# Kernel optimization log

Hardware: AMD Instinct MI355X
Metric: run time of the kernel (lower is better)

## Reference

```python
import jax, jax.numpy as jnp
import numpy as np

V, E, H, L, S, B = 32000, 512, 1024, 2, 512, 32


def setup_inputs() -> dict:
    key = jax.random.key(0)
    ks = jax.random.split(key, 12)
    s = 0.05  # keep activations in a sane range
    return {
        "x": jax.random.randint(ks[0], (S, B), 0, V),
        "embed": jax.random.normal(ks[1], (V, E), dtype=jnp.float32) * s,
        "W_ih0": jax.random.normal(ks[2], (4 * H, E), dtype=jnp.float32) * s,
        "W_hh0": jax.random.normal(ks[3], (4 * H, H), dtype=jnp.float32) * s,
        "b_ih0": jax.random.normal(ks[4], (4 * H,), dtype=jnp.float32) * s,
        "b_hh0": jax.random.normal(ks[5], (4 * H,), dtype=jnp.float32) * s,
        "W_ih1": jax.random.normal(ks[6], (4 * H, H), dtype=jnp.float32) * s,
        "W_hh1": jax.random.normal(ks[7], (4 * H, H), dtype=jnp.float32) * s,
        "b_ih1": jax.random.normal(ks[8], (4 * H,), dtype=jnp.float32) * s,
        "b_hh1": jax.random.normal(ks[9], (4 * H,), dtype=jnp.float32) * s,
        "h0": jax.random.normal(ks[10], (L, B, H), dtype=jnp.float32) * s,
        "c0": jax.random.normal(ks[11], (L, B, H), dtype=jnp.float32) * s,
    }


def _lstm_cell(x_t, h_prev, c_prev, Wi, Wh, bi, bh):
    # PyTorch gate order: input, forget, cell(g), output
    gates = x_t @ Wi.T + h_prev @ Wh.T + bi + bh  # [B, 4H]
    i, f, g, o = jnp.split(gates, 4, axis=-1)
    i = jax.nn.sigmoid(i)
    f = jax.nn.sigmoid(f)
    g = jnp.tanh(g)
    o = jax.nn.sigmoid(o)
    c_new = f * c_prev + i * g
    h_new = o * jnp.tanh(c_new)
    return h_new, c_new


def reference(x, embed, W_ih0, W_hh0, b_ih0, b_hh0,
              W_ih1, W_hh1, b_ih1, b_hh1, h0, c0):
    emb = embed[x]  # [S, B, E]; dropout p=0.0 -> identity
    layers = ((W_ih0, W_hh0, b_ih0, b_hh0), (W_ih1, W_hh1, b_ih1, b_hh1))

    def step(carry, e_t):
        h, c = carry  # each [L, B, H]
        inp = e_t
        new_h, new_c = [], []
        for l, (Wi, Wh, bi, bh) in enumerate(layers):
            h_l, c_l = _lstm_cell(inp, h[l], c[l], Wi, Wh, bi, bh)
            new_h.append(h_l)
            new_c.append(c_l)
            inp = h_l  # inter-layer dropout p=0.0 -> identity
        h = jnp.stack(new_h)
        c = jnp.stack(new_c)
        return (h, c), (inp, h, c)

    (_, _), (outs, hiddens, cells) = jax.lax.scan(step, (h0, c0), emb)
    outputs = outs[:, None, :, :]  # match torch shape [S, 1, B, H]
    return outputs, hiddens, cells
```

## Files before the change

kernel.cpp:

```cpp
#include <hip/hip_runtime.h>
#include <hip/hip_cooperative_groups.h>

namespace cg = cooperative_groups;


#define S_LEN 512
#define BATCH 32
#define HID   1024
#define EMB   512
#define NBLK  128
#define NTHR  512

typedef short  bf16x8 __attribute__((ext_vector_type(8)));
typedef float  f32x4  __attribute__((ext_vector_type(4)));

union U8 { bf16x8 v; unsigned short us[8]; uint4 u4; unsigned long long ull[2]; };

__device__ __forceinline__ unsigned short f2bf(float f) {
    unsigned u = __float_as_uint(f);
    u += 0x7fffu + ((u >> 16) & 1u);
    return (unsigned short)(u >> 16);
}

__device__ __forceinline__ uint4 pack8(float4 lo, float4 hi) {
    U8 r;
    r.us[0] = f2bf(lo.x); r.us[1] = f2bf(lo.y); r.us[2] = f2bf(lo.z); r.us[3] = f2bf(lo.w);
    r.us[4] = f2bf(hi.x); r.us[5] = f2bf(hi.y); r.us[6] = f2bf(hi.z); r.us[7] = f2bf(hi.w);
    return r.u4;
}

__device__ __forceinline__ f32x4 mfma16(bf16x8 a, bf16x8 b, f32x4 c) {
    return __builtin_amdgcn_mfma_f32_16x16x32_bf16(a, b, c, 0, 0, 0);
}

__device__ __forceinline__ U8 ld_ws16(const uint4* p) {
    const unsigned long long* q = (const unsigned long long*)p;
    U8 r;
    r.ull[0] = __hip_atomic_load(q,     __ATOMIC_RELAXED, __HIP_MEMORY_SCOPE_AGENT);
    r.ull[1] = __hip_atomic_load(q + 1, __ATOMIC_RELAXED, __HIP_MEMORY_SCOPE_AGENT);
    return r;
}
__device__ __forceinline__ void st_ws16(uint4* p, U8 v) {
    unsigned long long* q = (unsigned long long*)p;
    __hip_atomic_store(q,     v.ull[0], __ATOMIC_RELAXED, __HIP_MEMORY_SCOPE_AGENT);
    __hip_atomic_store(q + 1, v.ull[1], __ATOMIC_RELAXED, __HIP_MEMORY_SCOPE_AGENT);
}

__device__ __forceinline__ float sigm(float x) {
    return __builtin_amdgcn_rcpf(1.0f + __expf(-x));
}
__device__ __forceinline__ float tanh_fast(float x) {
    const float xc = fminf(fmaxf(x, -15.f), 15.f);
    const float t  = __expf(2.f * xc);
    return (t - 1.f) * __builtin_amdgcn_rcpf(t + 1.f);
}

__device__ __forceinline__ void poll64(const int* flags, int target) {
    const int* p = flags + ((threadIdx.x & 63) << 4);
    for (;;) {
        const int v = __hip_atomic_load(p, __ATOMIC_RELAXED, __HIP_MEMORY_SCOPE_AGENT);
        if (__all(v >= target)) break;
        __builtin_amdgcn_s_sleep(1);
    }
}

__global__ __launch_bounds__(NTHR, 1)
void lstm_pipe(const int* __restrict__ x, const float* __restrict__ embed,
               const float* __restrict__ Wi0, const float* __restrict__ Wh0,
               const float* __restrict__ bi0, const float* __restrict__ bh0,
               const float* __restrict__ Wi1, const float* __restrict__ Wh1,
               const float* __restrict__ bi1, const float* __restrict__ bh1,
               const float* __restrict__ h0in, const float* __restrict__ c0in,
               float* __restrict__ outputs, float* __restrict__ hiddens,
               float* __restrict__ cells, uint4* __restrict__ ws)
{
    __shared__ f32x4 sRed[8][8][64];
    __shared__ float sGates[32][68];
    __shared__ unsigned short sHex[32][16];
    __shared__ float sBias[16][4];
    uint4* sEmb = (uint4*)&sRed[0][0][0];

    const int tid  = threadIdx.x;
    const int lane = tid & 63;
    const int wv   = tid >> 6;
    const int bx   = blockIdx.x;
    const bool isL0 = (bx < 64);
    const int g    = isL0 ? bx : bx - 64;

    uint4* h0base = ws;
    uint4* h1base = ws + 16384;
    int*   fbase  = (int*)(ws + 24576);
    int*   flag0  = fbase;
    int*   flag1  = fbase + 1024;

    {
        const int gt = bx * NTHR + tid;
        if (gt < 2048) fbase[gt] = 0;
        if (gt < 8192) {
            const int layer = gt >> 12, kg = (gt >> 5) & 127, b = gt & 31;
            const float* src = h0in + (((size_t)layer << 5) + b) * HID + (kg << 3);
            uint4* dst = layer ? (h1base + 4096) : (h0base + 3 * 4096);
            dst[(kg << 5) + b] = pack8(*(const float4*)src, *(const float4*)(src + 4));
        }
    }
    if (tid < 16) {
        #pragma unroll
        for (int gate = 0; gate < 4; ++gate) {
            const int r = (gate << 10) + (g << 4) + tid;
            sBias[tid][gate] = isL0 ? (bi0[r] + bh0[r]) : (bi1[r] + bh1[r]);
        }
    }
    const int pjj = tid & 15;
    const int pb  = tid >> 4;
    const int jg  = (g << 4) + pjj;
    float creg = isL0 ? c0in[(size_t)pb * HID + jg]
                      : c0in[(size_t)(BATCH + pb) * HID + jg];

    const int n_    = lane & 15;
    const int ko_   = (lane >> 4) << 3;
    const int rb_   = ((n_ >> 2) << 10) + (g << 4) + (n_ & 3);
    bf16x8 w0[4][6];
    bf16x8 w1[4][8];
    if (isL0) {
        #pragma unroll
        for (int nt = 0; nt < 4; ++nt) {
            const int r = rb_ + (nt << 2);
            #pragma unroll
            for (int kf = 0; kf < 6; ++kf) {
                const int k = wv * 192 + kf * 32 + ko_;
                const float* src = (k < EMB) ? Wi0 + (size_t)r * EMB + k
                                             : Wh0 + (size_t)r * HID + (k - EMB);
                U8 t; t.u4 = pack8(*(const float4*)src, *(const float4*)(src + 4));
                w0[nt][kf] = t.v;
            }
        }
    } else {
        #pragma unroll
        for (int nt = 0; nt < 4; ++nt) {
            const int r = rb_ + (nt << 2);
            #pragma unroll
            for (int kf = 0; kf < 8; ++kf) {
                const int k = (wv << 8) + kf * 32 + ko_;
                const float* src = (k < HID) ? Wi1 + (size_t)r * HID + k
                                             : Wh1 + (size_t)r * HID + (k - HID);
                U8 t; t.u4 = pack8(*(const float4*)src, *(const float4*)(src + 4));
                w1[nt][kf] = t.v;
            }
        }
    }

    float4 pe[4][2];
    if (isL0) {
        #pragma unroll
        for (int it = 0; it < 4; ++it) {
            const int b = wv + (it << 3);
            const float* src = embed + (size_t)x[b] * EMB + (lane << 3);
            pe[it][0] = *(const float4*)src;
            pe[it][1] = *(const float4*)(src + 4);
        }
    }

    cg::grid_group grid = cg::this_grid();
    grid.sync();

    const size_t BH = (size_t)BATCH * HID;

    if (isL0) {
        for (int s = 0; s < S_LEN; ++s) {
            #pragma unroll
            for (int it = 0; it < 4; ++it)
                sEmb[lane * 33 + wv + (it << 3)] = pack8(pe[it][0], pe[it][1]);
            __syncthreads();

            if (s + 1 < S_LEN) {
                #pragma unroll
                for (int it = 0; it < 4; ++it) {
                    const int b = wv + (it << 3);
                    const float* src = embed + (size_t)x[((s + 1) << 5) + b] * EMB + (lane << 3);
                    pe[it][0] = *(const float4*)src;
                    pe[it][1] = *(const float4*)(src + 4);
                }
            }
            if (wv >= 2) poll64(flag0, s);

            const uint4* h0p = h0base + (((s + 3) & 3) << 12);

            U8 r0[6], r1[6];
            #pragma unroll
            for (int kf = 0; kf < 6; ++kf) {
                const int kfg = wv * 6 + kf;
                if (kfg >= 16) {
                    const int u = (((kfg - 16) << 2) + (lane >> 4)) * 32 + (lane & 15);
                    r0[kf] = ld_ws16(&h0p[u]);
                    r1[kf] = ld_ws16(&h0p[u + 16]);
                }
            }
            f32x4 acc[2][4] = {{{0,0,0,0},{0,0,0,0},{0,0,0,0},{0,0,0,0}},
                               {{0,0,0,0},{0,0,0,0},{0,0,0,0},{0,0,0,0}}};
            #pragma unroll
            for (int kf = 0; kf < 6; ++kf) {
                const int kfg = wv * 6 + kf;
                bf16x8 a0, a1;
                if (kfg < 16) {
                    const int u = ((kfg << 2) + (lane >> 4)) * 33 + (lane & 15);
                    U8 t0; t0.u4 = sEmb[u];      a0 = t0.v;
                    U8 t1; t1.u4 = sEmb[u + 16]; a1 = t1.v;
                } else {
                    a0 = r0[kf].v;
                    a1 = r1[kf].v;
                }
                #pragma unroll
                for (int nt = 0; nt < 4; ++nt) {
                    acc[0][nt] = mfma16(a0, w0[nt][kf], acc[0][nt]);
                    acc[1][nt] = mfma16(a1, w0[nt][kf], acc[1][nt]);
                }
            }
            __syncthreads();
            #pragma unroll
            for (int mt = 0; mt < 2; ++mt)
                #pragma unroll
                for (int nt = 0; nt < 4; ++nt)
                    sRed[wv][(mt << 2) + nt][lane] = acc[mt][nt];
            __syncthreads();
            {
                const int tile = tid >> 6, l = tid & 63;
                f32x4 sum = sRed[0][tile][l];
                #pragma unroll
                for (int w = 1; w < 8; ++w) sum += sRed[w][tile][l];
                const int mt = tile >> 2, nt = tile & 3;
                const int b0 = (mt << 4) + ((l >> 4) << 2);
                const int col = (nt << 4) + (l & 15);
                sGates[b0 + 0][col] = sum[0];
                sGates[b0 + 1][col] = sum[1];
                sGates[b0 + 2][col] = sum[2];
                sGates[b0 + 3][col] = sum[3];
            }
            __syncthreads();
            float cn_out, hn_out;
            {
                const int cb = ((pjj >> 2) << 4) + (pjj & 3);
                const float ii = sigm     (sGates[pb][cb]      + sBias[pjj][0]);
                const float ff = sigm     (sGates[pb][cb + 4]  + sBias[pjj][1]);
                const float gg = tanh_fast(sGates[pb][cb + 8]  + sBias[pjj][2]);
                const float oo = sigm     (sGates[pb][cb + 12] + sBias[pjj][3]);
                cn_out = ff * creg + ii * gg;
                creg = cn_out;
                hn_out = oo * tanh_fast(cn_out);
                sHex[pb][pjj] = f2bf(hn_out);
            }
            __syncthreads();
            if (wv == 0) {
                if (s >= 4) poll64(flag1, s - 3);
                const int b = lane & 31, kgl = lane >> 5;
                U8 hb;
                #pragma unroll
                for (int jj = 0; jj < 8; ++jj) hb.us[jj] = sHex[b][(kgl << 3) + jj];
                st_ws16(h0base + ((s & 3) << 12) + (((g << 1) + kgl) << 5) + b, hb);
                asm volatile("s_waitcnt vmcnt(0)" ::: "memory");
                if (lane == 0)
                    __hip_atomic_store(flag0 + (g << 4), s + 1,
                                       __ATOMIC_RELAXED, __HIP_MEMORY_SCOPE_AGENT);
            }
            cells  [(size_t)(s << 1) * BH + (size_t)pb * HID + jg] = cn_out;
            hiddens[(size_t)(s << 1) * BH + (size_t)pb * HID + jg] = hn_out;
        }
    } else {
        for (int s = 0; s < S_LEN; ++s) {
            if (wv < 4) poll64(flag0, s + 1);
            else        poll64(flag1, s);

            const uint4* h0c = h0base + ((s & 3) << 12);
            const uint4* h1p = h1base + (((s + 1) & 1) << 12);

            U8 r0[8], r1[8];
            #pragma unroll
            for (int kf = 0; kf < 8; ++kf) {
                const int kfg = (wv << 3) + kf;
                const uint4* src = (kfg < 32) ? h0c : h1p;
                const int u = (((kfg & 31) << 2) + (lane >> 4)) * 32 + (lane & 15);
                r0[kf] = ld_ws16(&src[u]);
                r1[kf] = ld_ws16(&src[u + 16]);
            }
            f32x4 acc[2][4] = {{{0,0,0,0},{0,0,0,0},{0,0,0,0},{0,0,0,0}},
                               {{0,0,0,0},{0,0,0,0},{0,0,0,0},{0,0,0,0}}};
            #pragma unroll
            for (int kf = 0; kf < 8; ++kf) {
                #pragma unroll
                for (int nt = 0; nt < 4; ++nt) {
                    acc[0][nt] = mfma16(r0[kf].v, w1[nt][kf], acc[0][nt]);
                    acc[1][nt] = mfma16(r1[kf].v, w1[nt][kf], acc[1][nt]);
                }
            }
            #pragma unroll
            for (int mt = 0; mt < 2; ++mt)
                #pragma unroll
                for (int nt = 0; nt < 4; ++nt)
                    sRed[wv][(mt << 2) + nt][lane] = acc[mt][nt];
            __syncthreads();
            {
                const int tile = tid >> 6, l = tid & 63;
                f32x4 sum = sRed[0][tile][l];
                #pragma unroll
                for (int w = 1; w < 8; ++w) sum += sRed[w][tile][l];
                const int mt = tile >> 2, nt = tile & 3;
                const int b0 = (mt << 4) + ((l >> 4) << 2);
                const int col = (nt << 4) + (l & 15);
                sGates[b0 + 0][col] = sum[0];
                sGates[b0 + 1][col] = sum[1];
                sGates[b0 + 2][col] = sum[2];
                sGates[b0 + 3][col] = sum[3];
            }
            __syncthreads();
            float cn_out, hn_out;
            {
                const int cb = ((pjj >> 2) << 4) + (pjj & 3);
                const float ii = sigm     (sGates[pb][cb]      + sBias[pjj][0]);
                const float ff = sigm     (sGates[pb][cb + 4]  + sBias[pjj][1]);
                const float gg = tanh_fast(sGates[pb][cb + 8]  + sBias[pjj][2]);
                const float oo = sigm     (sGates[pb][cb + 12] + sBias[pjj][3]);
                cn_out = ff * creg + ii * gg;
                creg = cn_out;
                hn_out = oo * tanh_fast(cn_out);
                sHex[pb][pjj] = f2bf(hn_out);
            }
            __syncthreads();
            if (wv == 0) {
                const int b = lane & 31, kgl = lane >> 5;
                U8 hb;
                #pragma unroll
                for (int jj = 0; jj < 8; ++jj) hb.us[jj] = sHex[b][(kgl << 3) + jj];
                st_ws16(h1base + ((s & 1) << 12) + (((g << 1) + kgl) << 5) + b, hb);
                asm volatile("s_waitcnt vmcnt(0)" ::: "memory");
                if (lane == 0)
                    __hip_atomic_store(flag1 + (g << 4), s + 1,
                                       __ATOMIC_RELAXED, __HIP_MEMORY_SCOPE_AGENT);
            }
            {
                const size_t o = (size_t)pb * HID + jg;
                cells  [(size_t)((s << 1) + 1) * BH + o] = cn_out;
                hiddens[(size_t)((s << 1) + 1) * BH + o] = hn_out;
                outputs[(size_t)s * BH + o]              = hn_out;
            }
        }
    }
}

#define KC 256
__global__ __launch_bounds__(256)
void lstm_step(const float* __restrict__ Wi, const float* __restrict__ Wh,
               const float* __restrict__ bi, const float* __restrict__ bh,
               const float* __restrict__ xsrc, const int* __restrict__ xidx, int K1,
               const float* __restrict__ Hprev, const float* __restrict__ Cprev,
               float* __restrict__ Hout, float* __restrict__ Cout,
               float* __restrict__ Hout2)
{
    __shared__ float As[32][KC + 4];
    __shared__ float red[256][5];

    const int t  = threadIdx.x;
    const int b  = t & 31;
    const int jl = (t >> 5) & 1;
    const int ks = t >> 6;
    const int j  = (blockIdx.x << 1) + jl;

    const int Ktot = K1 + HID;
    const int NC   = Ktot / KC;

    float acc0 = 0.f, acc1 = 0.f, acc2 = 0.f, acc3 = 0.f;

    for (int c = 0; c < NC; ++c) {
        const int  k0  = c * KC;
        const bool isX = (k0 < K1);

        #pragma unroll
        for (int i = 0; i < 8; ++i) {
            const int idx4 = t + (i << 8);
            const int row  = idx4 >> 6;
            const int c4   = idx4 & 63;
            const float* src;
            if (isX) {
                const size_t r0 = xidx ? (size_t)xidx[row] : (size_t)row;
                src = xsrc + r0 * (size_t)K1 + k0;
            } else {
                src = Hprev + (size_t)row * HID + (k0 - K1);
            }
            *(float4*)&As[row][c4 << 2] = *(const float4*)(src + (c4 << 2));
        }
        __syncthreads();

        const float* W      = isX ? Wi : Wh;
        const int    stride = isX ? K1 : HID;
        const int    kw     = k0 + (ks << 6) - (isX ? 0 : K1);
        const float* w0 = W + (size_t)(j       ) * stride + kw;
        const float* w1 = W + (size_t)(j + 1024) * stride + kw;
        const float* w2 = W + (size_t)(j + 2048) * stride + kw;
        const float* w3 = W + (size_t)(j + 3072) * stride + kw;
        const float* a  = &As[b][ks << 6];

        #pragma unroll 4
        for (int kk = 0; kk < 64; kk += 4) {
            const float4 av = *(const float4*)(a + kk);
            float4 w;
            w = *(const float4*)(w0 + kk);
            acc0 = fmaf(av.x, w.x, acc0); acc0 = fmaf(av.y, w.y, acc0);
            acc0 = fmaf(av.z, w.z, acc0); acc0 = fmaf(av.w, w.w, acc0);
            w = *(const float4*)(w1 + kk);
            acc1 = fmaf(av.x, w.x, acc1); acc1 = fmaf(av.y, w.y, acc1);
            acc1 = fmaf(av.z, w.z, acc1); acc1 = fmaf(av.w, w.w, acc1);
            w = *(const float4*)(w2 + kk);
            acc2 = fmaf(av.x, w.x, acc2); acc2 = fmaf(av.y, w.y, acc2);
            acc2 = fmaf(av.z, w.z, acc2); acc2 = fmaf(av.w, w.w, acc2);
            w = *(const float4*)(w3 + kk);
            acc3 = fmaf(av.x, w.x, acc3); acc3 = fmaf(av.y, w.y, acc3);
            acc3 = fmaf(av.z, w.z, acc3); acc3 = fmaf(av.w, w.w, acc3);
        }
        __syncthreads();
    }

    red[t][0] = acc0; red[t][1] = acc1; red[t][2] = acc2; red[t][3] = acc3;
    __syncthreads();

    if (t < 64) {
        float tot[4];
        #pragma unroll
        for (int gg = 0; gg < 4; ++gg) {
            const int r = j + (gg << 10);
            tot[gg] = red[t][gg] + red[t + 64][gg] + red[t + 128][gg] + red[t + 192][gg]
                   + bi[r] + bh[r];
        }
        const float ig = 1.f / (1.f + expf(-tot[0]));
        const float fg = 1.f / (1.f + expf(-tot[1]));
        const float gv = tanhf(tot[2]);
        const float og = 1.f / (1.f + expf(-tot[3]));
        const size_t o  = (size_t)b * HID + j;
        const float  cp = Cprev[o];
        const float  cn = fg * cp + ig * gv;
        const float  hn = og * tanhf(cn);
        Cout[o] = cn;
        Hout[o] = hn;
        if (Hout2) Hout2[o] = hn;
    }
}

extern "C" void kernel_launch(void* const* d_in, const int* in_sizes, int n_in,
                              void* d_out, int out_size, void* d_ws, size_t ws_size,
                              hipStream_t stream)
{
    (void)in_sizes; (void)n_in; (void)out_size;

    const int*   x     = (const int*)  d_in[0];
    const float* embed = (const float*)d_in[1];
    const float* Wi0   = (const float*)d_in[2];
    const float* Wh0   = (const float*)d_in[3];
    const float* bi0   = (const float*)d_in[4];
    const float* bh0   = (const float*)d_in[5];
    const float* Wi1   = (const float*)d_in[6];
    const float* Wh1   = (const float*)d_in[7];
    const float* bi1   = (const float*)d_in[8];
    const float* bh1   = (const float*)d_in[9];
    const float* h0in  = (const float*)d_in[10];
    const float* c0in  = (const float*)d_in[11];

    float* out     = (float*)d_out;
    const size_t BH = (size_t)BATCH * HID;
    float* outputs = out;
    float* hiddens = out + (size_t)S_LEN * BH;
    float* cells   = out + 3 * (size_t)S_LEN * BH;
    uint4* ws      = (uint4*)d_ws;

    bool coop_ok = (ws_size >= 401408);
    if (coop_ok) {
        void* args[] = {
            (void*)&x, (void*)&embed,
            (void*)&Wi0, (void*)&Wh0, (void*)&bi0, (void*)&bh0,
            (void*)&Wi1, (void*)&Wh1, (void*)&bi1, (void*)&bh1,
            (void*)&h0in, (void*)&c0in,
            (void*)&outputs, (void*)&hiddens, (void*)&cells, (void*)&ws
        };
        hipError_t e = hipLaunchCooperativeKernel((void*)lstm_pipe,
                                                  dim3(NBLK), dim3(NTHR), args, 0, stream);
        if (e != hipSuccess) { (void)hipGetLastError(); coop_ok = false; }
    }
    if (!coop_ok) {
        for (int s = 0; s < S_LEN; ++s) {
            const float* Hp0 = s ? hiddens + ((size_t)(s - 1) * 2 + 0) * BH : h0in;
            const float* Cp0 = s ? cells   + ((size_t)(s - 1) * 2 + 0) * BH : c0in;
            float* H0o = hiddens + ((size_t)s * 2 + 0) * BH;
            float* C0o = cells   + ((size_t)s * 2 + 0) * BH;
            lstm_step<<<512, 256, 0, stream>>>(Wi0, Wh0, bi0, bh0,
                                               embed, x + (size_t)s * BATCH, EMB,
                                               Hp0, Cp0, H0o, C0o, nullptr);

            const float* Hp1 = s ? hiddens + ((size_t)(s - 1) * 2 + 1) * BH : h0in + BH;
            const float* Cp1 = s ? cells   + ((size_t)(s - 1) * 2 + 1) * BH : c0in + BH;
            float* H1o = hiddens + ((size_t)s * 2 + 1) * BH;
            float* C1o = cells   + ((size_t)s * 2 + 1) * BH;
            lstm_step<<<512, 256, 0, stream>>>(Wi1, Wh1, bi1, bh1,
                                               H0o, nullptr, HID,
                                               Hp1, Cp1, H1o, C1o, outputs + (size_t)s * BH);
        }
    }
}
```

Measured before the change: 3.453 ms.

## Poll only producer subsets and double-buffer embedding staging in LSTM pipeline

Waves now poll only the flags of the producer blocks whose hidden-state slices they actually read, rather than waiting on all 64 producers. Embedding staging gets its own shared buffer and is prefetched two steps ahead, written after the reduction barrier, which removes one __syncthreads per layer-0 step. This is meant to shorten the per-timestep dependency chain on the serial recurrence, at the cost of extra shared memory and more intricate index logic for the subsets.

```diff
diff --git a/kernel.cpp b/kernel.cpp
--- a/kernel.cpp
+++ b/kernel.cpp
@@ -57,6 +57,16 @@
 
 __device__ __forceinline__ void poll64(const int* flags, int target) {
     const int* p = flags + ((threadIdx.x & 63) << 4);
+    for (;;) {
+        const int v = __hip_atomic_load(p, __ATOMIC_RELAXED, __HIP_MEMORY_SCOPE_AGENT);
+        if (__all(v >= target)) break;
+        __builtin_amdgcn_s_sleep(1);
+    }
+}
+__device__ __forceinline__ void pollsub(const int* flags, int base, int cnt, int target) {
+    const int l   = threadIdx.x & 63;
+    const int idx = (l < cnt) ? l : 0;
+    const int* p  = flags + ((base + idx) << 4);
     for (;;) {
         const int v = __hip_atomic_load(p, __ATOMIC_RELAXED, __HIP_MEMORY_SCOPE_AGENT);
         if (__all(v >= target)) break;
@@ -75,10 +85,10 @@
                float* __restrict__ cells, uint4* __restrict__ ws)
 {
     __shared__ f32x4 sRed[8][8][64];
+    __shared__ uint4 sEmb[64 * 33];
     __shared__ float sGates[32][68];
     __shared__ unsigned short sHex[32][16];
     __shared__ float sBias[16][4];
-    uint4* sEmb = (uint4*)&sRed[0][0][0];
 
     const int tid  = threadIdx.x;
     const int lane = tid & 63;
@@ -116,9 +126,9 @@
     float creg = isL0 ? c0in[(size_t)pb * HID + jg]
                       : c0in[(size_t)(BATCH + pb) * HID + jg];
 
-    const int n_    = lane & 15;
-    const int ko_   = (lane >> 4) << 3;
-    const int rb_   = ((n_ >> 2) << 10) + (g << 4) + (n_ & 3);
+    const int n_  = lane & 15;
+    const int ko_ = (lane >> 4) << 3;
+    const int rb_ = ((n_ >> 2) << 10) + (g << 4) + (n_ & 3);
     bf16x8 w0[4][6];
     bf16x8 w1[4][8];
     if (isL0) {
@@ -155,6 +165,12 @@
         for (int it = 0; it < 4; ++it) {
             const int b = wv + (it << 3);
             const float* src = embed + (size_t)x[b] * EMB + (lane << 3);
+            sEmb[lane * 33 + b] = pack8(*(const float4*)src, *(const float4*)(src + 4));
+        }
+        #pragma unroll
+        for (int it = 0; it < 4; ++it) {
+            const int b = wv + (it << 3);
+            const float* src = embed + (size_t)x[32 + b] * EMB + (lane << 3);
             pe[it][0] = *(const float4*)src;
             pe[it][1] = *(const float4*)(src + 4);
         }
@@ -167,32 +183,21 @@
 
     if (isL0) {
         for (int s = 0; s < S_LEN; ++s) {
-            #pragma unroll
-            for (int it = 0; it < 4; ++it)
-                sEmb[lane * 33 + wv + (it << 3)] = pack8(pe[it][0], pe[it][1]);
-            __syncthreads();
-
-            if (s + 1 < S_LEN) {
-                #pragma unroll
-                for (int it = 0; it < 4; ++it) {
-                    const int b = wv + (it << 3);
-                    const float* src = embed + (size_t)x[((s + 1) << 5) + b] * EMB + (lane << 3);
-                    pe[it][0] = *(const float4*)src;
-                    pe[it][1] = *(const float4*)(src + 4);
-                }
-            }
-            if (wv >= 2) poll64(flag0, s);
-
-            const uint4* h0p = h0base + (((s + 3) & 3) << 12);
-
             U8 r0[6], r1[6];
-            #pragma unroll
-            for (int kf = 0; kf < 6; ++kf) {
-                const int kfg = wv * 6 + kf;
-                if (kfg >= 16) {
-                    const int u = (((kfg - 16) << 2) + (lane >> 4)) * 32 + (lane & 15);
-                    r0[kf] = ld_ws16(&h0p[u]);
-                    r1[kf] = ld_ws16(&h0p[u + 16]);
+            if (wv >= 2) {
+                const int fst = (wv * 6 < 16) ? 16 : wv * 6;
+                const int pb0 = (fst - 16) << 1;
+                const int pct = ((wv * 6 + 6 - 16) << 1) - pb0;
+                pollsub(flag0, pb0, pct, s);
+                const uint4* h0p = h0base + (((s + 3) & 3) << 12);
+                #pragma unroll
+                for (int kf = 0; kf < 6; ++kf) {
+                    const int kfg = wv * 6 + kf;
+                    if (kfg >= 16) {
+                        const int u = (((kfg - 16) << 2) + (lane >> 4)) * 32 + (lane & 15);
+                        r0[kf] = ld_ws16(&h0p[u]);
+                        r1[kf] = ld_ws16(&h0p[u + 16]);
+                    }
                 }
             }
             f32x4 acc[2][4] = {{{0,0,0,0},{0,0,0,0},{0,0,0,0},{0,0,0,0}},
@@ -215,13 +220,27 @@
                     acc[1][nt] = mfma16(a1, w0[nt][kf], acc[1][nt]);
                 }
             }
-            __syncthreads();
             #pragma unroll
             for (int mt = 0; mt < 2; ++mt)
                 #pragma unroll
                 for (int nt = 0; nt < 4; ++nt)
                     sRed[wv][(mt << 2) + nt][lane] = acc[mt][nt];
             __syncthreads();
+
+            if (s + 1 < S_LEN) {
+                #pragma unroll
+                for (int it = 0; it < 4; ++it)
+                    sEmb[lane * 33 + wv + (it << 3)] = pack8(pe[it][0], pe[it][1]);
+            }
+            if (s + 2 < S_LEN) {
+                #pragma unroll
+                for (int it = 0; it < 4; ++it) {
+                    const int b = wv + (it << 3);
+                    const float* src = embed + (size_t)x[((s + 2) << 5) + b] * EMB + (lane << 3);
+                    pe[it][0] = *(const float4*)src;
+                    pe[it][1] = *(const float4*)(src + 4);
+                }
+            }
             {
                 const int tile = tid >> 6, l = tid & 63;
                 f32x4 sum = sRed[0][tile][l];
@@ -236,6 +255,7 @@
                 sGates[b0 + 3][col] = sum[3];
             }
             __syncthreads();
+
             float cn_out, hn_out;
             {
                 const int cb = ((pjj >> 2) << 4) + (pjj & 3);
@@ -249,6 +269,7 @@
                 sHex[pb][pjj] = f2bf(hn_out);
             }
             __syncthreads();
+
             if (wv == 0) {
                 if (s >= 4) poll64(flag1, s - 3);
                 const int b = lane & 31, kgl = lane >> 5;
@@ -266,12 +287,11 @@
         }
     } else {
         for (int s = 0; s < S_LEN; ++s) {
-            if (wv < 4) poll64(flag0, s + 1);
+            if (wv < 4) pollsub(flag0, wv << 4, 16, s + 1);
             else        poll64(flag1, s);
 
             const uint4* h0c = h0base + ((s & 3) << 12);
             const uint4* h1p = h1base + (((s + 1) & 1) << 12);
-
             U8 r0[8], r1[8];
             #pragma unroll
             for (int kf = 0; kf < 8; ++kf) {
```

Result: faster. 3.361 ms (-2.7%).
